# Performance work log

Hardware: AMD Instinct MI355X
Metric: run time of the kernel (lower is better)

Reference implementation:

```python
import jax, jax.numpy as jnp
import numpy as np

L = 16384      # sequence length
CH = 512       # input channels
S = 128        # SSM state dim


def setup_inputs() -> dict:
    key = jax.random.key(0)
    kx, kb, kc, kdt = jax.random.split(key, 4)
    x = jax.random.normal(kx, (L, CH), dtype=jnp.float32)
    # logA init matches flax param init: log(1 + arange(state_dim))
    logA = jnp.log(1.0 + jnp.arange(S, dtype=jnp.float32))
    # Dense (no bias) kernels, lecun-normal-ish scale 1/sqrt(fan_in)
    scale = 1.0 / np.sqrt(CH)
    WB = jax.random.normal(kb, (CH, S), dtype=jnp.float32) * scale
    WC = jax.random.normal(kc, (CH, S), dtype=jnp.float32) * scale
    Wdt = jax.random.normal(kdt, (CH, 1), dtype=jnp.float32) * scale
    bdt = jnp.zeros((1,), dtype=jnp.float32)
    return {"x": x, "logA": logA, "WB": WB, "WC": WC, "Wdt": Wdt, "bdt": bdt}


def reference(x, logA, WB, WC, Wdt, bdt):
    A = -jnp.exp(logA)                      # (S,)
    B = x @ WB                              # (L, S)
    C = x @ WC                              # (L, S)
    dt = jax.nn.softplus(x @ Wdt + bdt)     # (L, 1), learned since dt=None
    Abar = jnp.exp(A * dt)                  # (L, S) discretized transition
    Bbar = (Abar - 1.0) * B / A             # (L, S) discretized input term

    def scan_fn(el1, el2):
        (A1, B1), (A2, B2) = el1, el2
        return (A1 * A2, A1 * B2)           # faithful to source (non-standard combine)

    _, AkB = jax.lax.associative_scan(scan_fn, (Abar, Bbar))  # over axis 0 (L)
    return jnp.einsum('ls,ls,lc->lc', C, AkB, x)              # (L, CH)
```

## Files before the change

### kernel.cpp

```cpp
#include <hip/hip_runtime.h>
#include <math.h>

#define L_SEQ  16384
#define CHN    512
#define S_DIM  128
#define NPRE   1024
#define E_CUT  104.0f

static __device__ __forceinline__ float softplus_f(float z) {
    return (z > 20.f) ? z : log1pf(expf(z));
}

__global__ __launch_bounds__(256) void k_dt(const float* __restrict__ x,
                                            const float* __restrict__ Wdt,
                                            const float* __restrict__ bdt,
                                            float* __restrict__ dt)
{
    const int wave = threadIdx.x >> 6;
    const int lane = threadIdx.x & 63;
    const int row  = blockIdx.x * 4 + wave;

    const float4* xr = (const float4*)(x + (size_t)row * CHN);
    const float4* w4 = (const float4*)Wdt;

    float acc = 0.f;
#pragma unroll
    for (int i = 0; i < 2; ++i) {
        float4 xv = xr[lane + 64 * i];
        float4 wv = w4[lane + 64 * i];
        acc = fmaf(xv.x, wv.x, acc);
        acc = fmaf(xv.y, wv.y, acc);
        acc = fmaf(xv.z, wv.z, acc);
        acc = fmaf(xv.w, wv.w, acc);
    }
#pragma unroll
    for (int off = 32; off; off >>= 1) acc += __shfl_down(acc, off);

    if (lane == 0) dt[row] = softplus_f(acc + bdt[0]);
}

__global__ __launch_bounds__(64) void k_scan_fb(const float* __restrict__ x,
                                                const float* __restrict__ Wdt,
                                                const float* __restrict__ bdt,
                                                float* __restrict__ dt,
                                                float* __restrict__ E,
                                                int*   __restrict__ n_p)
{
    const int lane = threadIdx.x;
    const int PER  = NPRE / 64;

    float v[PER], ex[PER];
    const float4* dt4 = (const float4*)dt;
#pragma unroll
    for (int i = 0; i < PER / 4; ++i) {
        float4 q = dt4[lane * (PER / 4) + i];
        v[4*i+0] = q.x; v[4*i+1] = q.y; v[4*i+2] = q.z; v[4*i+3] = q.w;
    }

    float run = 0.f;
#pragma unroll
    for (int i = 0; i < PER; ++i) { ex[i] = run; run += v[i]; }

    float incl = run;
#pragma unroll
    for (int off = 1; off < 64; off <<= 1) {
        float o = __shfl_up(incl, off);
        if (lane >= off) incl += o;
    }
    const float excl  = incl - run;
    const float total = __shfl(incl, 63);

    float4* E4 = (float4*)E;
#pragma unroll
    for (int i = 0; i < PER / 4; ++i)
        E4[lane * (PER / 4) + i] = make_float4(excl + ex[4*i],   excl + ex[4*i+1],
                                               excl + ex[4*i+2], excl + ex[4*i+3]);

    int cnt = 0;
#pragma unroll
    for (int i = 0; i < PER; ++i) cnt += (excl + ex[i] < E_CUT) ? 1 : 0;
#pragma unroll
    for (int off = 32; off; off >>= 1) cnt += __shfl_down(cnt, off);
    int n = __shfl(cnt, 0);

    if (n == NPRE) {
        float running = total;
        for (int l = NPRE; l < L_SEQ && running < E_CUT; ++l) {
            const float4* xr = (const float4*)(x + (size_t)l * CHN);
            const float4* w4 = (const float4*)Wdt;
            float acc = 0.f;
#pragma unroll
            for (int i = 0; i < 2; ++i) {
                float4 xv = xr[lane + 64 * i];
                float4 wv = w4[lane + 64 * i];
                acc = fmaf(xv.x, wv.x, acc); acc = fmaf(xv.y, wv.y, acc);
                acc = fmaf(xv.z, wv.z, acc); acc = fmaf(xv.w, wv.w, acc);
            }
#pragma unroll
            for (int off = 32; off; off >>= 1) acc += __shfl_down(acc, off);
            float d = softplus_f(__shfl(acc, 0) + bdt[0]);
            if (lane == 0) { E[l] = running; dt[l] = d; }
            running += d;
            ++n;
        }
    }
    if (lane == 0) n_p[0] = n;
}

__global__ __launch_bounds__(256) void k_out(const float* __restrict__ x,
                                             const float* __restrict__ logA,
                                             const float* __restrict__ WB,
                                             const float* __restrict__ WC,
                                             const float* __restrict__ dt,
                                             const float* __restrict__ E,
                                             const int* __restrict__ n_p,
                                             float* __restrict__ out)
{
    const int n  = n_p[0];
    const int t  = threadIdx.x;
    const int g  = t >> 5;
    const int s4 = t & 31;

    __shared__ float  xs[CHN];
    __shared__ float4 redB[8][32];
    __shared__ float4 redC[8][32];
    __shared__ float  scal;

    const float4* wb = (const float4*)WB;
    const float4* wc = (const float4*)WC;

    for (int l = blockIdx.x; l < L_SEQ; l += gridDim.x) {
        float* orow = out + (size_t)l * CHN;

        if (l >= n) {
            ((float2*)orow)[t] = make_float2(0.f, 0.f);
            continue;
        }

        ((float2*)xs)[t] = ((const float2*)(x + (size_t)l * CHN))[t];
        __syncthreads();

        float4 aB = make_float4(0.f, 0.f, 0.f, 0.f);
        float4 aC = make_float4(0.f, 0.f, 0.f, 0.f);
#pragma unroll 8
        for (int c = g; c < CHN; c += 8) {
            const float  xc = xs[c];
            const float4 b  = wb[c * 32 + s4];
            const float4 cc = wc[c * 32 + s4];
            aB.x = fmaf(xc, b.x,  aB.x);  aB.y = fmaf(xc, b.y,  aB.y);
            aB.z = fmaf(xc, b.z,  aB.z);  aB.w = fmaf(xc, b.w,  aB.w);
            aC.x = fmaf(xc, cc.x, aC.x);  aC.y = fmaf(xc, cc.y, aC.y);
            aC.z = fmaf(xc, cc.z, aC.z);  aC.w = fmaf(xc, cc.w, aC.w);
        }
        redB[g][s4] = aB;
        redC[g][s4] = aC;
        __syncthreads();

        if (t < 32) {
            float4 B = redB[0][t], C = redC[0][t];
#pragma unroll
            for (int k = 1; k < 8; ++k) {
                float4 b = redB[k][t], c = redC[k][t];
                B.x += b.x; B.y += b.y; B.z += b.z; B.w += b.w;
                C.x += c.x; C.y += c.y; C.z += c.z; C.w += c.w;
            }
            const float  e   = E[l];
            const float  dtl = dt[l];
            const float4 la  = ((const float4*)logA)[t];

            float con = 0.f;
            {
                float a = -expf(la.x);
                con = fmaf(C.x * expf(a * e), expm1f(a * dtl) * B.x / a, con);
                a = -expf(la.y);
                con = fmaf(C.y * expf(a * e), expm1f(a * dtl) * B.y / a, con);
                a = -expf(la.z);
                con = fmaf(C.z * expf(a * e), expm1f(a * dtl) * B.z / a, con);
                a = -expf(la.w);
                con = fmaf(C.w * expf(a * e), expm1f(a * dtl) * B.w / a, con);
            }
#pragma unroll
            for (int off = 16; off; off >>= 1) con += __shfl_down(con, off);
            if (t == 0) scal = con;
        }
        __syncthreads();

        const float  sc = scal;
        const float2 xv = ((float2*)xs)[t];
        ((float2*)orow)[t] = make_float2(sc * xv.x, sc * xv.y);
        __syncthreads();
    }
}

extern "C" void kernel_launch(void* const* d_in, const int* in_sizes, int n_in,
                              void* d_out, int out_size, void* d_ws, size_t ws_size,
                              hipStream_t stream)
{
    const float* x    = (const float*)d_in[0];
    const float* logA = (const float*)d_in[1];
    const float* WB   = (const float*)d_in[2];
    const float* WC   = (const float*)d_in[3];
    const float* Wdt  = (const float*)d_in[4];
    const float* bdt  = (const float*)d_in[5];
    float* out = (float*)d_out;

    float* dt  = (float*)d_ws;
    float* E   = dt + L_SEQ;
    int*   n_p = (int*)(E + L_SEQ);

    k_dt     <<<NPRE / 4, 256, 0, stream>>>(x, Wdt, bdt, dt);
    k_scan_fb<<<1,        64,  0, stream>>>(x, Wdt, bdt, dt, E, n_p);
    k_out    <<<2048,     256, 0, stream>>>(x, logA, WB, WC, dt, E, n_p, out);
}
```

Measured before the change: 35.20 us.

## Move output zero-fill into first dt kernel and shrink active-row kernel grid

The 32 MB zero-fill of the output moves out of the final kernel and into the first kernel, which also computes dt for the prefix rows, so it runs before the serial single-wave scan rather than after it. The final kernel now loops only over the active rows (l < n), and its grid drops from 2048 to 256 blocks. The aim is to take the bulk output write off the critical path after the scan and to stop launching blocks that only write zeros. The catch is that the first kernel becomes much heavier, and the fewer blocks each handle more active rows serially.

```diff
diff --git a/kernel.cpp b/kernel.cpp
--- a/kernel.cpp
+++ b/kernel.cpp
@@ -5,38 +5,50 @@
 #define CHN    512
 #define S_DIM  128
 #define NPRE   1024
+#define FBLK   2048
 #define E_CUT  104.0f
 
 static __device__ __forceinline__ float softplus_f(float z) {
     return (z > 20.f) ? z : log1pf(expf(z));
 }
 
-__global__ __launch_bounds__(256) void k_dt(const float* __restrict__ x,
-                                            const float* __restrict__ Wdt,
-                                            const float* __restrict__ bdt,
-                                            float* __restrict__ dt)
-{
-    const int wave = threadIdx.x >> 6;
-    const int lane = threadIdx.x & 63;
-    const int row  = blockIdx.x * 4 + wave;
-
-    const float4* xr = (const float4*)(x + (size_t)row * CHN);
-    const float4* w4 = (const float4*)Wdt;
-
-    float acc = 0.f;
-#pragma unroll
-    for (int i = 0; i < 2; ++i) {
-        float4 xv = xr[lane + 64 * i];
-        float4 wv = w4[lane + 64 * i];
-        acc = fmaf(xv.x, wv.x, acc);
-        acc = fmaf(xv.y, wv.y, acc);
-        acc = fmaf(xv.z, wv.z, acc);
-        acc = fmaf(xv.w, wv.w, acc);
-    }
-#pragma unroll
-    for (int off = 32; off; off >>= 1) acc += __shfl_down(acc, off);
-
-    if (lane == 0) dt[row] = softplus_f(acc + bdt[0]);
+__global__ __launch_bounds__(256) void k_fill_dt(const float* __restrict__ x,
+                                                 const float* __restrict__ Wdt,
+                                                 const float* __restrict__ bdt,
+                                                 float* __restrict__ dt,
+                                                 float* __restrict__ out)
+{
+    const int b = blockIdx.x;
+    const int t = threadIdx.x;
+
+    {
+        float4* o4 = (float4*)out;
+        const float4 z = make_float4(0.f, 0.f, 0.f, 0.f);
+        size_t i = (size_t)b * 256 + t;
+#pragma unroll
+        for (int k = 0; k < 4; ++k) {
+            o4[i] = z;
+            i += (size_t)FBLK * 256;
+        }
+    }
+
+    if (b < NPRE / 4) {
+        const int wave = t >> 6, lane = t & 63;
+        const int row  = b * 4 + wave;
+        const float4* xr = (const float4*)(x + (size_t)row * CHN);
+        const float4* w4 = (const float4*)Wdt;
+        float acc = 0.f;
+#pragma unroll
+        for (int i = 0; i < 2; ++i) {
+            float4 xv = xr[lane + 64 * i];
+            float4 wv = w4[lane + 64 * i];
+            acc = fmaf(xv.x, wv.x, acc); acc = fmaf(xv.y, wv.y, acc);
+            acc = fmaf(xv.z, wv.z, acc); acc = fmaf(xv.w, wv.w, acc);
+        }
+#pragma unroll
+        for (int off = 32; off; off >>= 1) acc += __shfl_down(acc, off);
+        if (lane == 0) dt[row] = softplus_f(acc + bdt[0]);
+    }
 }
 
 __global__ __launch_bounds__(64) void k_scan_fb(const float* __restrict__ x,
@@ -107,14 +119,14 @@
     if (lane == 0) n_p[0] = n;
 }
 
-__global__ __launch_bounds__(256) void k_out(const float* __restrict__ x,
-                                             const float* __restrict__ logA,
-                                             const float* __restrict__ WB,
-                                             const float* __restrict__ WC,
-                                             const float* __restrict__ dt,
-                                             const float* __restrict__ E,
-                                             const int* __restrict__ n_p,
-                                             float* __restrict__ out)
+__global__ __launch_bounds__(256) void k_active(const float* __restrict__ x,
+                                                const float* __restrict__ logA,
+                                                const float* __restrict__ WB,
+                                                const float* __restrict__ WC,
+                                                const float* __restrict__ dt,
+                                                const float* __restrict__ E,
+                                                const int* __restrict__ n_p,
+                                                float* __restrict__ out)
 {
     const int n  = n_p[0];
     const int t  = threadIdx.x;
@@ -129,14 +141,7 @@
     const float4* wb = (const float4*)WB;
     const float4* wc = (const float4*)WC;
 
-    for (int l = blockIdx.x; l < L_SEQ; l += gridDim.x) {
-        float* orow = out + (size_t)l * CHN;
-
-        if (l >= n) {
-            ((float2*)orow)[t] = make_float2(0.f, 0.f);
-            continue;
-        }
-
+    for (int l = blockIdx.x; l < n; l += gridDim.x) {
         ((float2*)xs)[t] = ((const float2*)(x + (size_t)l * CHN))[t];
         __syncthreads();
 
@@ -145,12 +150,12 @@
 #pragma unroll 8
         for (int c = g; c < CHN; c += 8) {
             const float  xc = xs[c];
-            const float4 b  = wb[c * 32 + s4];
-            const float4 cc = wc[c * 32 + s4];
-            aB.x = fmaf(xc, b.x,  aB.x);  aB.y = fmaf(xc, b.y,  aB.y);
-            aB.z = fmaf(xc, b.z,  aB.z);  aB.w = fmaf(xc, b.w,  aB.w);
-            aC.x = fmaf(xc, cc.x, aC.x);  aC.y = fmaf(xc, cc.y, aC.y);
-            aC.z = fmaf(xc, cc.z, aC.z);  aC.w = fmaf(xc, cc.w, aC.w);
+            const float4 bq = wb[c * 32 + s4];
+            const float4 cq = wc[c * 32 + s4];
+            aB.x = fmaf(xc, bq.x, aB.x);  aB.y = fmaf(xc, bq.y, aB.y);
+            aB.z = fmaf(xc, bq.z, aB.z);  aB.w = fmaf(xc, bq.w, aB.w);
+            aC.x = fmaf(xc, cq.x, aC.x);  aC.y = fmaf(xc, cq.y, aC.y);
+            aC.z = fmaf(xc, cq.z, aC.z);  aC.w = fmaf(xc, cq.w, aC.w);
         }
         redB[g][s4] = aB;
         redC[g][s4] = aC;
@@ -160,25 +165,23 @@
             float4 B = redB[0][t], C = redC[0][t];
 #pragma unroll
             for (int k = 1; k < 8; ++k) {
-                float4 b = redB[k][t], c = redC[k][t];
-                B.x += b.x; B.y += b.y; B.z += b.z; B.w += b.w;
-                C.x += c.x; C.y += c.y; C.z += c.z; C.w += c.w;
+                float4 bq = redB[k][t], cq = redC[k][t];
+                B.x += bq.x; B.y += bq.y; B.z += bq.z; B.w += bq.w;
+                C.x += cq.x; C.y += cq.y; C.z += cq.z; C.w += cq.w;
             }
             const float  e   = E[l];
             const float  dtl = dt[l];
             const float4 la  = ((const float4*)logA)[t];
 
             float con = 0.f;
-            {
-                float a = -expf(la.x);
-                con = fmaf(C.x * expf(a * e), expm1f(a * dtl) * B.x / a, con);
-                a = -expf(la.y);
-                con = fmaf(C.y * expf(a * e), expm1f(a * dtl) * B.y / a, con);
-                a = -expf(la.z);
-                con = fmaf(C.z * expf(a * e), expm1f(a * dtl) * B.z / a, con);
-                a = -expf(la.w);
-                con = fmaf(C.w * expf(a * e), expm1f(a * dtl) * B.w / a, con);
-            }
+            float a = -expf(la.x);
+            con = fmaf(C.x * expf(a * e), expm1f(a * dtl) * B.x / a, con);
+            a = -expf(la.y);
+            con = fmaf(C.y * expf(a * e), expm1f(a * dtl) * B.y / a, con);
+            a = -expf(la.z);
+            con = fmaf(C.z * expf(a * e), expm1f(a * dtl) * B.z / a, con);
+            a = -expf(la.w);
+            con = fmaf(C.w * expf(a * e), expm1f(a * dtl) * B.w / a, con);
 #pragma unroll
             for (int off = 16; off; off >>= 1) con += __shfl_down(con, off);
             if (t == 0) scal = con;
@@ -187,7 +190,7 @@
 
         const float  sc = scal;
         const float2 xv = ((float2*)xs)[t];
-        ((float2*)orow)[t] = make_float2(sc * xv.x, sc * xv.y);
+        ((float2*)(out + (size_t)l * CHN))[t] = make_float2(sc * xv.x, sc * xv.y);
         __syncthreads();
     }
 }
@@ -208,7 +211,7 @@
     float* E   = dt + L_SEQ;
     int*   n_p = (int*)(E + L_SEQ);
 
-    k_dt     <<<NPRE / 4, 256, 0, stream>>>(x, Wdt, bdt, dt);
-    k_scan_fb<<<1,        64,  0, stream>>>(x, Wdt, bdt, dt, E, n_p);
-    k_out    <<<2048,     256, 0, stream>>>(x, logA, WB, WC, dt, E, n_p, out);
-}
+    k_fill_dt<<<FBLK, 256, 0, stream>>>(x, Wdt, bdt, dt, out);
+    k_scan_fb<<<1,    64,  0, stream>>>(x, Wdt, bdt, dt, E, n_p);
+    k_active <<<256,  256, 0, stream>>>(x, logA, WB, WC, dt, E, n_p, out);
+}
```

Result: faster. 34.50 us (-2.0%).
